# Kernel tuning notes

Measured on AMD Instinct MI355X. Metric: run time of the kernel, lower is better.

Reference implementation:

```python
import jax, jax.numpy as jnp
import numpy as np

B, CIN, COUT, G, HEADS = 4, 256, 256, 8, 4
K, S, P = 7, 1, 3
H = W = 32
IN_W = CIN // G
OUT_W = COUT // G


def setup_inputs() -> dict:
    key = jax.random.key(0)
    ks = jax.random.split(key, 9)
    def n(k, shape, scale=1.0):
        return jax.random.normal(k, shape, dtype=jnp.float32) * scale
    # kaiming fan_out init for the 1x1 convs (fan_out = out channels)
    return {
        "x": n(ks[0], (B, CIN, H, W)),
        "wq": n(ks[1], (G, OUT_W * HEADS, IN_W), (2.0 / (OUT_W * HEADS)) ** 0.5),
        "bq": n(ks[2], (G, OUT_W * HEADS), 0.01),
        "wk": n(ks[3], (G, OUT_W, IN_W), (2.0 / OUT_W) ** 0.5),
        "bk": n(ks[4], (G, OUT_W), 0.01),
        "wv": n(ks[5], (G, OUT_W, IN_W), (2.0 / OUT_W) ** 0.5),
        "bv": n(ks[6], (G, OUT_W), 0.01),
        "rel_h": n(ks[7], (OUT_W // 2, 1, 1, G, K, 1)),
        "rel_w": n(ks[8], (OUT_W // 2, 1, 1, G, 1, K)),
    }


def _sparse_conv(x, w, b):
    # grouped 1x1 conv, groups stacked on last axis (matches torch.stack(dim=-1))
    # x: [B, G*I, h, w]; w: [G, O, I]; b: [G, O] -> [B, O, h, w, G]
    Bn, C, hh, ww = x.shape
    xr = x.reshape(Bn, G, C // G, hh, ww)
    out = jnp.einsum('bgihw,goi->bohwg', xr, w)
    return out + b.T[None, :, None, None, :]


def _unfold(x5, k, s):
    # x5: [B, C, Hp, Wp, G] -> [B, C, Ho, Wo, G, k, k]  (torch unfold(2).unfold(3))
    Bn, C, Hp, Wp, Gn = x5.shape
    Ho = (Hp - k) // s + 1
    Wo = (Wp - k) // s + 1
    patches = jnp.stack(
        [x5[:, :, i:i + (Ho - 1) * s + 1:s, j:j + (Wo - 1) * s + 1:s, :]
         for i in range(k) for j in range(k)], axis=-1)
    return patches.reshape(Bn, C, Ho, Wo, Gn, k, k)


def reference(x, wq, bq, wk, bk, wv, bv, rel_h, rel_w):
    xp = jnp.pad(x, ((0, 0), (0, 0), (P, P), (P, P)))
    q = _sparse_conv(x, wq, bq)    # [B, OUT_W*HEADS, H, W, G]
    k = _sparse_conv(xp, wk, bk)   # [B, OUT_W, Hp, Wp, G] (bias at padded locations, as in torch)
    v = _sparse_conv(xp, wv, bv)
    k = _unfold(k, K, S)           # [B, OUT_W, H, W, G, K, K]
    v = _unfold(v, K, S)
    kh, kw = jnp.split(k, 2, axis=1)
    k = jnp.concatenate([kh + rel_h, kw + rel_w], axis=1)
    kf = k.reshape(B, OUT_W, H, W, G * K * K)
    vf = v.reshape(B, OUT_W, H, W, G * K * K)
    q = q.reshape(B, HEADS, OUT_W, H, W, G)
    # scores: sum over channel c; softmax over flattened (group, kh, kw) window
    scores = jnp.einsum('bhcxyg,bcxym->bhxygm', q, kf)
    attn = jax.nn.softmax(scores, axis=-1)
    # weighted sum over window m and heads h (matches sum(dim=1) then sum(dim=-1))
    out = jnp.einsum('bhxygm,bcxym->bcxyg', attn, vf)   # [B, OUT_W, H, W, G]
    out = jnp.transpose(out, (0, 4, 2, 3, 1)).reshape(B, -1, H, W)  # transpose(1,-1)+reshape
    return out
```

## Files before the change

kernel.cpp:

```cpp
#include <hip/hip_runtime.h>
#include <math.h>

typedef _Float16 f16;
typedef _Float16 f16x4 __attribute__((ext_vector_type(4)));
typedef _Float16 f16x8 __attribute__((ext_vector_type(8)));
typedef __bf16 bf16x2 __attribute__((ext_vector_type(2)));
typedef __bf16 bf16x4 __attribute__((ext_vector_type(4)));
typedef __bf16 bf16x4a4 __attribute__((ext_vector_type(4), aligned(4)));
typedef short s16x4 __attribute__((ext_vector_type(4)));
typedef short s16x4a4 __attribute__((ext_vector_type(4), aligned(4)));
typedef float f32x4 __attribute__((ext_vector_type(4)));

#define MFMA_F16(a, b, c)  __builtin_amdgcn_mfma_f32_16x16x32_f16(a, b, c, 0, 0, 0)
#define MFMA_BF16_K16(a, b, c) __builtin_amdgcn_mfma_f32_16x16x16bf16_1k(a, b, c, 0, 0, 0)

static __device__ inline f16x8 cvt8(const float* p) {
    const float4* p4 = (const float4*)p;
    float4 u0 = p4[0], u1 = p4[1];
    f16x8 r;
    r[0] = (f16)u0.x; r[1] = (f16)u0.y; r[2] = (f16)u0.z; r[3] = (f16)u0.w;
    r[4] = (f16)u1.x; r[5] = (f16)u1.y; r[6] = (f16)u1.z; r[7] = (f16)u1.w;
    return r;
}

__global__ __launch_bounds__(256) void produce_kernel(
    const float* __restrict__ x,
    const float* __restrict__ wq, const float* __restrict__ bq,
    const float* __restrict__ wk, const float* __restrict__ bk,
    const float* __restrict__ wv, const float* __restrict__ bv,
    const float* __restrict__ rel_h, const float* __restrict__ rel_w,
    f16* __restrict__ Qb, f16* __restrict__ Kb,
    __bf16* __restrict__ VtA, __bf16* __restrict__ VtB,
    f16* __restrict__ relp) {
    int bid = blockIdx.x;
    int t = threadIdx.x;

    if (bid == 1216) {
        for (int idx = t; idx < 448 * 32; idx += 256) {
            int c = idx & 31, key = idx >> 5;
            int kw = key & 7, ghk = key >> 3;
            int gp = (ghk * 37) >> 8;
            int kh = ghk - gp * 7;
            float v = 0.f;
            if (kw < 7)
                v = (c < 16) ? rel_h[c * 56 + gp * 7 + kh]
                             : rel_w[(c - 16) * 56 + gp * 7 + kw];
            relp[idx] = (f16)v;
        }
        return;
    }

    int hp = bid % 38, g = (bid / 38) & 7, b = bid / 304;
    bool hin = (hp >= 3 && hp < 35);
    size_t kvbase = (size_t)(b * 8 + g);

    if (!hin) {
        for (int idx = t; idx < 38 * 32; idx += 256) {
            int wp = idx >> 5, c = idx & 31;
            Kb[((kvbase * 38 + hp) * 38 + wp) * 32 + c] = (f16)bk[g * 32 + c];
        }
        for (int idx = t; idx < 40 * 32; idx += 256) {
            int i = idx >> 5, c = idx & 31;
            size_t vo = ((kvbase * 32 + c) * 38 + hp) * 40;
            __bf16 bb = (__bf16)bv[g * 32 + c];
            VtA[vo + i] = (i < 38) ? bb : (__bf16)0.f;
            VtB[vo + i] = (i < 37) ? bb : (__bf16)0.f;
        }
        return;
    }

    int h = hp - 3;
    __shared__ __align__(16) f16 xTl[32 * 40];

    {
        int ic = t >> 3, w = (t & 7) * 4;
        float4 xv = *(const float4*)(x + (((size_t)b * 256 + g * 32 + ic) * 32 + h) * 32 + w);
        xTl[(w + 0) * 40 + ic] = (f16)xv.x;
        xTl[(w + 1) * 40 + ic] = (f16)xv.y;
        xTl[(w + 2) * 40 + ic] = (f16)xv.z;
        xTl[(w + 3) * 40 + ic] = (f16)xv.w;
    }
    __syncthreads();

    int l15 = t & 15, quad = (t >> 4) & 3, wave = t >> 6;

    f16x8 xf0 = *(const f16x8*)(xTl + l15 * 40 + quad * 8);
    f16x8 xf1 = *(const f16x8*)(xTl + (16 + l15) * 40 + quad * 8);

#pragma unroll
    for (int i = 0; i < 2; ++i) {
        int mq = wave * 2 + i;
        f16x8 wf = cvt8(wq + ((size_t)g * 128 + mq * 16 + l15) * 32 + quad * 8);
        float4 b4 = *(const float4*)(bq + g * 128 + mq * 16 + quad * 4);
#pragma unroll
        for (int Nt = 0; Nt < 2; ++Nt) {
            f32x4 d = {0.f, 0.f, 0.f, 0.f};
            d = MFMA_F16(wf, Nt ? xf1 : xf0, d);
            f16x4 q4;
            q4[0] = (f16)(d[0] + b4.x); q4[1] = (f16)(d[1] + b4.y);
            q4[2] = (f16)(d[2] + b4.z); q4[3] = (f16)(d[3] + b4.w);
            int w = Nt * 16 + l15;
            *(f16x4*)(Qb + (size_t)((b * 32 + h) * 32 + w) * 1024 + g * 128 + mq * 16 + quad * 4) = q4;
        }
    }

    if (wave < 2) {
        f16x8 wf = cvt8(wk + ((size_t)g * 32 + wave * 16 + l15) * 32 + quad * 8);
        float4 b4 = *(const float4*)(bk + g * 32 + wave * 16 + quad * 4);
#pragma unroll
        for (int Nt = 0; Nt < 2; ++Nt) {
            f32x4 d = {0.f, 0.f, 0.f, 0.f};
            d = MFMA_F16(wf, Nt ? xf1 : xf0, d);
            f16x4 k4;
            k4[0] = (f16)(d[0] + b4.x); k4[1] = (f16)(d[1] + b4.y);
            k4[2] = (f16)(d[2] + b4.z); k4[3] = (f16)(d[3] + b4.w);
            int wp = Nt * 16 + l15 + 3;
            *(f16x4*)(Kb + ((kvbase * 38 + hp) * 38 + wp) * 32 + wave * 16 + quad * 4) = k4;
        }
    } else {
        int Nt = wave - 2;
        f16x8 wf = cvt8(wv + ((size_t)g * 32 + Nt * 16 + l15) * 32 + quad * 8);
        float bias = bv[g * 32 + Nt * 16 + l15];
        int c = Nt * 16 + l15;
        size_t vo = ((kvbase * 32 + c) * 38 + hp) * 40;
#pragma unroll
        for (int Mt = 0; Mt < 2; ++Mt) {
            f32x4 d = {0.f, 0.f, 0.f, 0.f};
            d = MFMA_F16(Mt ? xf1 : xf0, wf, d);
            __bf16 v0 = (__bf16)(d[0] + bias), v1 = (__bf16)(d[1] + bias);
            __bf16 v2 = (__bf16)(d[2] + bias), v3 = (__bf16)(d[3] + bias);
            int wp0 = Mt * 16 + quad * 4 + 3;
            VtA[vo + wp0] = v0;
            bf16x2 mid; mid[0] = v1; mid[1] = v2;
            *(bf16x2*)(VtA + vo + wp0 + 1) = mid;
            VtA[vo + wp0 + 3] = v3;
            bf16x4a4 p4; p4[0] = v0; p4[1] = v1; p4[2] = v2; p4[3] = v3;
            *(bf16x4a4*)(VtB + vo + wp0 - 1) = p4;
        }
    }

    for (int idx = t; idx < 192; idx += 256) {
        int wi = idx >> 5, c = idx & 31;
        int wp = (wi < 3) ? wi : (32 + wi);
        Kb[((kvbase * 38 + hp) * 38 + wp) * 32 + c] = (f16)bk[g * 32 + c];
        size_t vo = ((kvbase * 32 + c) * 38 + hp) * 40;
        __bf16 bb = (__bf16)bv[g * 32 + c];
        VtA[vo + wp] = bb;
        if (wp >= 1) VtB[vo + wp - 1] = bb;
    }
    for (int idx = t; idx < 160; idx += 256) {
        int c = idx / 5, j = idx % 5;
        size_t vo = ((kvbase * 32 + c) * 38 + hp) * 40;
        if (j < 2) VtA[vo + 38 + j] = (__bf16)0.f;
        else       VtB[vo + 35 + j] = (__bf16)0.f;
    }
}

__global__ __launch_bounds__(128, 4) void attn_kernel(
    const f16* __restrict__ Qb, const f16* __restrict__ Kb,
    const __bf16* __restrict__ VtA, const __bf16* __restrict__ VtB,
    const f16* __restrict__ relp, float* __restrict__ out) {
    int bid = blockIdx.x;
    int t = threadIdx.x;
    int wvi = t >> 6;
    int pid = ((bid & 7) * 256 + (bid >> 3)) * 2 + wvi;
    int y = pid & 31, x = (pid >> 5) & 31, b = pid >> 10;

    int lane = t & 63;
    int l15 = lane & 15, quad = lane >> 4, kwl = lane & 7, p8 = (lane >> 3) & 1;
    bool oddq = (quad & 1);
    int kw0 = (quad & 1) * 4;
    int gph = quad >> 1;

    f16x8 qf[2];
    {
        const f16* qp = Qb + (size_t)pid * 1024;
        qf[0] = *(const f16x8*)(qp + l15 * 32 + quad * 8);
        qf[1] = *(const f16x8*)(qp + (16 + l15) * 32 + quad * 8);
    }

    float fsumT[2] = {0.f, 0.f};
    f32x4 acc[2][2];
#pragma unroll
    for (int ct = 0; ct < 2; ++ct)
#pragma unroll
        for (int m = 0; m < 2; ++m) acc[ct][m] = (f32x4){0.f, 0.f, 0.f, 0.f};

    int yk = y + kwl;
    if (yk > 37) yk = 37;
    const __bf16* __restrict__ Vsel = (y & 1) ? VtB : VtA;
    int yv = (y & ~1) + kw0;

    for (int chunk = 0; chunk < 4; ++chunk) {
        int gpr = chunk * 2 + p8;
        int gpv = chunk * 2 + gph;
        const f16* kbp = Kb + ((((size_t)(b * 8 + gpr) * 38 + x) * 38 + yk) << 5) + quad * 8;
        const f16* rpp = relp + ((size_t)(gpr * 56 + kwl) << 5) + quad * 8;
        const __bf16* vp0 = Vsel + (((size_t)(b * 8 + gpv) * 32 + l15) * 38 + x) * 40 + yv;
        const __bf16* vp1 = vp0 + (size_t)16 * 38 * 40;
#pragma unroll
        for (int kh = 0; kh < 7; ++kh) {
            f16x8 kb = *(const f16x8*)kbp;  kbp += 38 * 32;
            f16x8 rp = *(const f16x8*)rpp;  rpp += 256;
            kb += rp;
            s16x4a4 vf0 = *(const s16x4a4*)vp0;  vp0 += 40;
            s16x4a4 vf1 = *(const s16x4a4*)vp1;  vp1 += 40;
#pragma unroll
            for (int Mt = 0; Mt < 2; ++Mt) {
                f32x4 d = {0.f, 0.f, 0.f, 0.f};
                d = MFMA_F16(kb, qf[Mt], d);
                float e0 = __expf(d[0]);
                float e1 = __expf(d[1]);
                float e2 = __expf(d[2]);
                float e3 = oddq ? 0.f : __expf(d[3]);
                fsumT[Mt] += (e0 + e1) + (e2 + e3);
                bf16x4 pb;
                pb[0] = (__bf16)e0; pb[1] = (__bf16)e1;
                pb[2] = (__bf16)e2; pb[3] = (__bf16)e3;
                s16x4 pbi = __builtin_bit_cast(s16x4, pb);
                acc[0][Mt] = MFMA_BF16_K16((s16x4)vf0, pbi, acc[0][Mt]);
                acc[1][Mt] = MFMA_BF16_K16((s16x4)vf1, pbi, acc[1][Mt]);
            }
        }
    }

#pragma unroll
    for (int m = 0; m < 2; ++m) {
        fsumT[m] += __shfl_xor(fsumT[m], 16);
        fsumT[m] += __shfl_xor(fsumT[m], 32);
    }
    float inv[2] = {1.0f / fsumT[0], 1.0f / fsumT[1]};

#pragma unroll
    for (int Mt = 0; Mt < 2; ++Mt)
#pragma unroll
        for (int ct = 0; ct < 2; ++ct) {
            float v[4];
#pragma unroll
            for (int r = 0; r < 4; ++r) {
                v[r] = acc[ct][Mt][r] * inv[Mt];
                v[r] += __shfl_xor(v[r], 1);
                v[r] += __shfl_xor(v[r], 2);
            }
            if ((l15 & 3) == 0) {
                int g = Mt * 4 + (l15 >> 2);
                float4 o4 = {v[0], v[1], v[2], v[3]};
                *(float4*)(out + ((((size_t)(b * 8 + g) * 32 + x) * 32 + y) << 5) +
                           ct * 16 + quad * 4) = o4;
            }
        }
}

extern "C" void kernel_launch(void* const* d_in, const int* in_sizes, int n_in,
                              void* d_out, int out_size, void* d_ws, size_t ws_size,
                              hipStream_t stream) {
    const float* x     = (const float*)d_in[0];
    const float* wq    = (const float*)d_in[1];
    const float* bq    = (const float*)d_in[2];
    const float* wk    = (const float*)d_in[3];
    const float* bk    = (const float*)d_in[4];
    const float* wv    = (const float*)d_in[5];
    const float* bv    = (const float*)d_in[6];
    const float* rel_h = (const float*)d_in[7];
    const float* rel_w = (const float*)d_in[8];
    float* out = (float*)d_out;

    unsigned char* ws = (unsigned char*)d_ws;
    f16*    Qb   = (f16*)ws;
    f16*    Kb   = (f16*)(ws + 8388608);
    __bf16* VtA  = (__bf16*)(ws + 8388608 + 2957312);
    __bf16* VtB  = (__bf16*)(ws + 8388608 + 2957312 + 3112960);
    f16*    relp = (f16*)(ws + 8388608 + 2957312 + 3112960 + 3112960);

    hipLaunchKernelGGL(produce_kernel, dim3(1217), dim3(256), 0, stream,
                       x, wq, bq, wk, bk, wv, bv, rel_h, rel_w, Qb, Kb, VtA, VtB, relp);
    hipLaunchKernelGGL(attn_kernel, dim3(2048), dim3(128), 0, stream,
                       Qb, Kb, VtA, VtB, relp, out);
}
```

Before: 130.0 us.

## Use four shifted channel-interleaved V copies and split chunks across two waves

The V tensor is now stored as four copies, each shifted by 0-3 columns and interleaved in blocks of four channels. Every attention lane can then do one aligned 8-byte load instead of a 4-byte-aligned 4-wide load from one of two shifted copies. The attention kernel also gives each pixel to two waves, each handling half of the group chunks, and sums the partial accumulators through shared memory. Twice as many blocks are launched. The price is twice the V producer writes and footprint, an extra barrier and LDS reduction, and half the waves exiting early at the epilogue.

```diff
diff --git a/kernel.cpp b/kernel.cpp
--- a/kernel.cpp
+++ b/kernel.cpp
@@ -6,13 +6,14 @@
 typedef _Float16 f16x8 __attribute__((ext_vector_type(8)));
 typedef __bf16 bf16x2 __attribute__((ext_vector_type(2)));
 typedef __bf16 bf16x4 __attribute__((ext_vector_type(4)));
-typedef __bf16 bf16x4a4 __attribute__((ext_vector_type(4), aligned(4)));
+typedef __bf16 bf16x4a8 __attribute__((ext_vector_type(4), aligned(8)));
 typedef short s16x4 __attribute__((ext_vector_type(4)));
-typedef short s16x4a4 __attribute__((ext_vector_type(4), aligned(4)));
 typedef float f32x4 __attribute__((ext_vector_type(4)));
 
 #define MFMA_F16(a, b, c)  __builtin_amdgcn_mfma_f32_16x16x32_f16(a, b, c, 0, 0, 0)
 #define MFMA_BF16_K16(a, b, c) __builtin_amdgcn_mfma_f32_16x16x16bf16_1k(a, b, c, 0, 0, 0)
+
+#define VSS 12160
 
 static __device__ inline f16x8 cvt8(const float* p) {
     const float4* p4 = (const float4*)p;
@@ -30,8 +31,7 @@
     const float* __restrict__ wv, const float* __restrict__ bv,
     const float* __restrict__ rel_h, const float* __restrict__ rel_w,
     f16* __restrict__ Qb, f16* __restrict__ Kb,
-    __bf16* __restrict__ VtA, __bf16* __restrict__ VtB,
-    f16* __restrict__ relp) {
+    __bf16* __restrict__ V4, f16* __restrict__ relp) {
     int bid = blockIdx.x;
     int t = threadIdx.x;
 
@@ -53,18 +53,18 @@
     int hp = bid % 38, g = (bid / 38) & 7, b = bid / 304;
     bool hin = (hp >= 3 && hp < 35);
     size_t kvbase = (size_t)(b * 8 + g);
+    size_t rowp = (kvbase * 38 + hp) * 10;
 
     if (!hin) {
         for (int idx = t; idx < 38 * 32; idx += 256) {
             int wp = idx >> 5, c = idx & 31;
             Kb[((kvbase * 38 + hp) * 38 + wp) * 32 + c] = (f16)bk[g * 32 + c];
         }
-        for (int idx = t; idx < 40 * 32; idx += 256) {
-            int i = idx >> 5, c = idx & 31;
-            size_t vo = ((kvbase * 32 + c) * 38 + hp) * 40;
-            __bf16 bb = (__bf16)bv[g * 32 + c];
-            VtA[vo + i] = (i < 38) ? bb : (__bf16)0.f;
-            VtB[vo + i] = (i < 37) ? bb : (__bf16)0.f;
+        for (int idx = t; idx < 4 * 40 * 32; idx += 256) {
+            int c = idx & 31, w = (idx >> 5) % 40, s = (idx >> 5) / 40;
+            int wp = s + w;
+            __bf16 val = (wp <= 37) ? (__bf16)bv[g * 32 + c] : (__bf16)0.f;
+            V4[((size_t)s * VSS + rowp + (w >> 2)) * 128 + c * 4 + (w & 3)] = val;
         }
         return;
     }
@@ -122,20 +122,22 @@
         f16x8 wf = cvt8(wv + ((size_t)g * 32 + Nt * 16 + l15) * 32 + quad * 8);
         float bias = bv[g * 32 + Nt * 16 + l15];
         int c = Nt * 16 + l15;
-        size_t vo = ((kvbase * 32 + c) * 38 + hp) * 40;
 #pragma unroll
         for (int Mt = 0; Mt < 2; ++Mt) {
             f32x4 d = {0.f, 0.f, 0.f, 0.f};
             d = MFMA_F16(Mt ? xf1 : xf0, wf, d);
             __bf16 v0 = (__bf16)(d[0] + bias), v1 = (__bf16)(d[1] + bias);
             __bf16 v2 = (__bf16)(d[2] + bias), v3 = (__bf16)(d[3] + bias);
-            int wp0 = Mt * 16 + quad * 4 + 3;
-            VtA[vo + wp0] = v0;
-            bf16x2 mid; mid[0] = v1; mid[1] = v2;
-            *(bf16x2*)(VtA + vo + wp0 + 1) = mid;
-            VtA[vo + wp0 + 3] = v3;
-            bf16x4a4 p4; p4[0] = v0; p4[1] = v1; p4[2] = v2; p4[3] = v3;
-            *(bf16x4a4*)(VtB + vo + wp0 - 1) = p4;
+            int p0 = Mt * 4 + quad;
+            __bf16* P0 = V4 + ((size_t)0 * VSS + rowp + p0) * 128 + c * 4;
+            __bf16* P1 = V4 + ((size_t)1 * VSS + rowp + p0) * 128 + c * 4;
+            __bf16* P2 = V4 + ((size_t)2 * VSS + rowp + p0) * 128 + c * 4;
+            __bf16* P3 = V4 + ((size_t)3 * VSS + rowp + p0) * 128 + c * 4;
+            { bf16x4a8 q; q[0] = v0; q[1] = v1; q[2] = v2; q[3] = v3; *(bf16x4a8*)P3 = q; }
+            { P2[1] = v0; bf16x2 m; m[0] = v1; m[1] = v2; *(bf16x2*)(P2 + 2) = m; P2[128] = v3; }
+            { bf16x2 m; m[0] = v0; m[1] = v1; *(bf16x2*)(P1 + 2) = m;
+              bf16x2 n; n[0] = v2; n[1] = v3; *(bf16x2*)(P1 + 128) = n; }
+            { P0[3] = v0; bf16x2 m; m[0] = v1; m[1] = v2; *(bf16x2*)(P0 + 128) = m; P0[130] = v3; }
         }
     }
 
@@ -143,34 +145,39 @@
         int wi = idx >> 5, c = idx & 31;
         int wp = (wi < 3) ? wi : (32 + wi);
         Kb[((kvbase * 38 + hp) * 38 + wp) * 32 + c] = (f16)bk[g * 32 + c];
-        size_t vo = ((kvbase * 32 + c) * 38 + hp) * 40;
-        __bf16 bb = (__bf16)bv[g * 32 + c];
-        VtA[vo + wp] = bb;
-        if (wp >= 1) VtB[vo + wp - 1] = bb;
-    }
-    for (int idx = t; idx < 160; idx += 256) {
-        int c = idx / 5, j = idx % 5;
-        size_t vo = ((kvbase * 32 + c) * 38 + hp) * 40;
-        if (j < 2) VtA[vo + 38 + j] = (__bf16)0.f;
-        else       VtB[vo + 35 + j] = (__bf16)0.f;
+    }
+    for (int idx = t; idx < 4 * 6 * 32; idx += 256) {
+        int c = idx & 31, wi = (idx >> 5) % 6, s = (idx >> 5) / 6;
+        int wp = (wi < 3) ? wi : (32 + wi);
+        if (wp >= s) {
+            int w = wp - s;
+            V4[((size_t)s * VSS + rowp + (w >> 2)) * 128 + c * 4 + (w & 3)] =
+                (__bf16)bv[g * 32 + c];
+        }
+    }
+    for (int idx = t; idx < 4 * 5 * 32; idx += 256) {
+        int c = idx & 31, j = (idx >> 5) % 5, s = (idx >> 5) / 5;
+        int w = 35 + j;
+        if (s + w >= 38)
+            V4[((size_t)s * VSS + rowp + (w >> 2)) * 128 + c * 4 + (w & 3)] = (__bf16)0.f;
     }
 }
 
 __global__ __launch_bounds__(128, 4) void attn_kernel(
     const f16* __restrict__ Qb, const f16* __restrict__ Kb,
-    const __bf16* __restrict__ VtA, const __bf16* __restrict__ VtB,
-    const f16* __restrict__ relp, float* __restrict__ out) {
+    const __bf16* __restrict__ V4, const f16* __restrict__ relp,
+    float* __restrict__ out) {
     int bid = blockIdx.x;
     int t = threadIdx.x;
     int wvi = t >> 6;
-    int pid = ((bid & 7) * 256 + (bid >> 3)) * 2 + wvi;
+    int pid = (bid & 7) * 512 + (bid >> 3);
     int y = pid & 31, x = (pid >> 5) & 31, b = pid >> 10;
+
+    __shared__ __align__(16) float accS[64 * 20];
 
     int lane = t & 63;
     int l15 = lane & 15, quad = lane >> 4, kwl = lane & 7, p8 = (lane >> 3) & 1;
     bool oddq = (quad & 1);
-    int kw0 = (quad & 1) * 4;
-    int gph = quad >> 1;
 
     f16x8 qf[2];
     {
@@ -188,23 +195,25 @@
 
     int yk = y + kwl;
     if (yk > 37) yk = 37;
-    const __bf16* __restrict__ Vsel = (y & 1) ? VtB : VtA;
-    int yv = (y & ~1) + kw0;
-
-    for (int chunk = 0; chunk < 4; ++chunk) {
+    int s = y & 3;
+    size_t vshift = (size_t)s * VSS;
+
+    for (int chunk = wvi * 2; chunk < wvi * 2 + 2; ++chunk) {
         int gpr = chunk * 2 + p8;
-        int gpv = chunk * 2 + gph;
+        int gpv = chunk * 2 + (quad >> 1);
         const f16* kbp = Kb + ((((size_t)(b * 8 + gpr) * 38 + x) * 38 + yk) << 5) + quad * 8;
         const f16* rpp = relp + ((size_t)(gpr * 56 + kwl) << 5) + quad * 8;
-        const __bf16* vp0 = Vsel + (((size_t)(b * 8 + gpv) * 32 + l15) * 38 + x) * 40 + yv;
-        const __bf16* vp1 = vp0 + (size_t)16 * 38 * 40;
+        const __bf16* vp0 = V4 +
+            ((vshift + ((size_t)(b * 8 + gpv) * 38 + x) * 10 + (y >> 2) + (quad & 1)) << 7) +
+            l15 * 4;
+        const __bf16* vp1 = vp0 + 64;
 #pragma unroll
         for (int kh = 0; kh < 7; ++kh) {
             f16x8 kb = *(const f16x8*)kbp;  kbp += 38 * 32;
             f16x8 rp = *(const f16x8*)rpp;  rpp += 256;
             kb += rp;
-            s16x4a4 vf0 = *(const s16x4a4*)vp0;  vp0 += 40;
-            s16x4a4 vf1 = *(const s16x4a4*)vp1;  vp1 += 40;
+            s16x4 vf0 = *(const s16x4*)vp0;  vp0 += 1280;
+            s16x4 vf1 = *(const s16x4*)vp1;  vp1 += 1280;
 #pragma unroll
             for (int Mt = 0; Mt < 2; ++Mt) {
                 f32x4 d = {0.f, 0.f, 0.f, 0.f};
@@ -218,8 +227,8 @@
                 pb[0] = (__bf16)e0; pb[1] = (__bf16)e1;
                 pb[2] = (__bf16)e2; pb[3] = (__bf16)e3;
                 s16x4 pbi = __builtin_bit_cast(s16x4, pb);
-                acc[0][Mt] = MFMA_BF16_K16((s16x4)vf0, pbi, acc[0][Mt]);
-                acc[1][Mt] = MFMA_BF16_K16((s16x4)vf1, pbi, acc[1][Mt]);
+                acc[0][Mt] = MFMA_BF16_K16(vf0, pbi, acc[0][Mt]);
+                acc[1][Mt] = MFMA_BF16_K16(vf1, pbi, acc[1][Mt]);
             }
         }
     }
@@ -228,6 +237,28 @@
     for (int m = 0; m < 2; ++m) {
         fsumT[m] += __shfl_xor(fsumT[m], 16);
         fsumT[m] += __shfl_xor(fsumT[m], 32);
+    }
+
+    if (wvi == 1) {
+        float* sp = accS + lane * 20;
+        *(f32x4*)(sp + 0)  = acc[0][0];
+        *(f32x4*)(sp + 4)  = acc[0][1];
+        *(f32x4*)(sp + 8)  = acc[1][0];
+        *(f32x4*)(sp + 12) = acc[1][1];
+        sp[16] = fsumT[0];
+        sp[17] = fsumT[1];
+    }
+    __syncthreads();
+    if (wvi == 1) return;
+
+    {
+        const float* sp = accS + lane * 20;
+        acc[0][0] += *(const f32x4*)(sp + 0);
+        acc[0][1] += *(const f32x4*)(sp + 4);
+        acc[1][0] += *(const f32x4*)(sp + 8);
+        acc[1][1] += *(const f32x4*)(sp + 12);
+        fsumT[0] += sp[16];
+        fsumT[1] += sp[17];
     }
     float inv[2] = {1.0f / fsumT[0], 1.0f / fsumT[1]};
 
@@ -268,12 +299,11 @@
     unsigned char* ws = (unsigned char*)d_ws;
     f16*    Qb   = (f16*)ws;
     f16*    Kb   = (f16*)(ws + 8388608);
-    __bf16* VtA  = (__bf16*)(ws + 8388608 + 2957312);
-    __bf16* VtB  = (__bf16*)(ws + 8388608 + 2957312 + 3112960);
-    f16*    relp = (f16*)(ws + 8388608 + 2957312 + 3112960 + 3112960);
+    __bf16* V4   = (__bf16*)(ws + 8388608 + 2957312);
+    f16*    relp = (f16*)(ws + 8388608 + 2957312 + 12451840);
 
     hipLaunchKernelGGL(produce_kernel, dim3(1217), dim3(256), 0, stream,
-                       x, wq, bq, wk, bk, wv, bv, rel_h, rel_w, Qb, Kb, VtA, VtB, relp);
-    hipLaunchKernelGGL(attn_kernel, dim3(2048), dim3(128), 0, stream,
-                       Qb, Kb, VtA, VtB, relp, out);
+                       x, wq, bq, wk, bk, wv, bv, rel_h, rel_w, Qb, Kb, V4, relp);
+    hipLaunchKernelGGL(attn_kernel, dim3(4096), dim3(128), 0, stream,
+                       Qb, Kb, V4, relp, out);
 }
```

Result: faster. 120.1 us (-7.6%).
